# Kernel optimization log

Hardware: AMD Instinct MI355X
Metric: run time of the kernel (lower is better)

Reference implementation:

```python
import jax, jax.numpy as jnp
import numpy as np

IGNORE_INDEX = 255


def setup_inputs() -> dict:
    key = jax.random.key(0)
    k1, k2 = jax.random.split(key)
    n, h, w = 8, 256, 256
    num_class, cnum = 20, 4
    c = num_class * cnum
    P = 8192  # number of parcel segments
    features = jax.random.normal(k1, (n, c, h, w), dtype=jnp.float32)
    parcel = jax.random.randint(k2, (n, h, w), 0, P, dtype=jnp.int32)
    # all pixels of a parcel share one class label (as the torch code assumes)
    target = (parcel % num_class).astype(jnp.int32)
    return {"features": features, "target": target, "parcel": parcel,
            "num_segments": P, "cnum": cnum, "num_class": num_class}


def reference(features, target, parcel, num_segments, cnum, num_class):
    n, c, h, w = features.shape
    hw = h * w
    # n c h w -> n (h w) c
    fea = features.reshape(n, c, hw).transpose(0, 2, 1)
    # MaxPool1d(cnum, stride=cnum) over channel dim: group consecutive cnum channels
    branch_dis = fea.reshape(n, hw, num_class, cnum).max(axis=-1)  # [n, hw, num_class]
    branch_dis = branch_dis.reshape(n * hw, num_class)

    t = target.reshape(-1)
    p = parcel.reshape(-1)
    valid = t != IGNORE_INDEX
    wgt = valid.astype(branch_dis.dtype)

    # fused segment-mean replacing the python loop over unique parcel ids
    seg_sum = jax.ops.segment_sum(branch_dis * wgt[:, None], p, num_segments=num_segments)
    counts = jax.ops.segment_sum(wgt, p, num_segments=num_segments)
    seg_mean = seg_sum / jnp.maximum(counts, 1.0)[:, None]  # [P, num_class]

    # per-parcel target (labels are constant within a parcel -> max == first)
    t_masked = jnp.where(valid, t, -1)
    tgt_parcel = jax.ops.segment_max(t_masked, p, num_segments=num_segments)
    seg_valid = (counts > 0).astype(seg_mean.dtype)

    logp = jax.nn.log_softmax(seg_mean, axis=-1)
    tgt_safe = jnp.clip(tgt_parcel, 0, num_class - 1)
    nll = -jnp.take_along_axis(logp, tgt_safe[:, None], axis=1)[:, 0]
    loss_dis = jnp.sum(nll * seg_valid) / jnp.maximum(jnp.sum(seg_valid), 1.0)

    # diversity branch: softmax over spatial dim, channel-group maxpool
    branch_div = jax.nn.softmax(fea, axis=1)  # softmax over hw
    branch_div = branch_div.reshape(n, hw, num_class, cnum).max(axis=-1)
    loss_div = 1.0 - jnp.mean(jnp.sum(branch_div, axis=1)) / num_class
    return loss_dis, loss_div
```

## Files before the change

kernel.cpp:

```cpp
#include <hip/hip_runtime.h>
#include <float.h>

#define IGNORE_INDEX 255

constexpr int N_IMG = 8;
constexpr int C     = 80;
constexpr int HW    = 65536;
constexpr int NC    = 20;
constexpr int CNUM  = 4;
constexpr int P     = 8192;
constexpr int NPIX  = N_IMG * HW;
constexpr int STRIPES = 4;
constexpr int NCH   = N_IMG * C;
constexpr int ROWB  = 48;

constexpr size_t B_BDS   = 0;
constexpr size_t B_CNT   = (size_t)NPIX * ROWB;
constexpr size_t B_ACC   = B_CNT + (size_t)P * 4;
constexpr size_t B_OFF   = B_ACC + 64;
constexpr size_t B_WOFF  = B_OFF + (size_t)P * 4;
constexpr size_t B_PS    = B_WOFF + (size_t)P * 4;
constexpr size_t B_CHOFF = B_PS + (size_t)NCH * STRIPES * 4;
constexpr size_t B_TGT   = B_CHOFF + (size_t)NCH * 4;

typedef __fp16 h2v __attribute__((ext_vector_type(2)));
__device__ __forceinline__ unsigned pkh(float a, float b) {
  h2v r = __builtin_amdgcn_cvt_pkrtz(a, b);
  return __builtin_bit_cast(unsigned, r);
}
__device__ __forceinline__ void unpkh(unsigned u, float& lo, float& hi) {
  h2v r = __builtin_bit_cast(h2v, u);
  lo = (float)r.x;
  hi = (float)r.y;
}
__device__ __forceinline__ float waveSum(float v) {
#pragma unroll
  for (int o = 32; o > 0; o >>= 1) v += __shfl_down(v, o, 64);
  return v;
}

__global__ __launch_bounds__(256) void stats_hist_kernel(
    const float* __restrict__ f, const int* __restrict__ target,
    const int* __restrict__ parcel, float* __restrict__ ps,
    int* __restrict__ cnt) {
  if (blockIdx.x >= NCH * STRIPES) {
    const int t4 = (blockIdx.x - NCH * STRIPES) * 256 + threadIdx.x;
    const int4 tv = ((const int4*)target)[t4];
    const int4 pv = ((const int4*)parcel)[t4];
    if (tv.x != IGNORE_INDEX) atomicAdd(&cnt[pv.x], 1);
    if (tv.y != IGNORE_INDEX) atomicAdd(&cnt[pv.y], 1);
    if (tv.z != IGNORE_INDEX) atomicAdd(&cnt[pv.z], 1);
    if (tv.w != IGNORE_INDEX) atomicAdd(&cnt[pv.w], 1);
    return;
  }
  const int ch = blockIdx.x >> 2, stripe = blockIdx.x & 3;
  const float4* base =
      (const float4*)(f + (size_t)ch * HW + (size_t)stripe * (HW / STRIPES));
  const int n4 = HW / STRIPES / 4;
  float s = 0.f;
  for (int i = threadIdx.x; i < n4; i += 256) {
    float4 v = base[i];
    s += __expf(v.x) + __expf(v.y) + __expf(v.z) + __expf(v.w);
  }
  __shared__ float sred[4];
  const int wid = threadIdx.x >> 6, lid = threadIdx.x & 63;
  float wsv = waveSum(s);
  if (lid == 0) sred[wid] = wsv;
  __syncthreads();
  if (threadIdx.x == 0)
    ps[blockIdx.x] = sred[0] + sred[1] + sred[2] + sred[3];
}

__global__ __launch_bounds__(1024) void combine_scan_kernel(
    const float* __restrict__ ps, float* __restrict__ choff,
    const int* __restrict__ cnt, int* __restrict__ offs,
    int* __restrict__ woff) {
  const int t = threadIdx.x;
  const int lid = t & 63, wid = t >> 6;
  if (t < NCH) {
    const float4 s4 = *(const float4*)(ps + t * 4);
    choff[t] = logf(s4.x + s4.y + s4.z + s4.w);
  }
  int4 a = ((const int4*)cnt)[t * 2], b = ((const int4*)cnt)[t * 2 + 1];
  int c[8] = {a.x, a.y, a.z, a.w, b.x, b.y, b.z, b.w};
  int tot = 0;
#pragma unroll
  for (int j = 0; j < 8; j++) tot += c[j];
  int x = tot;
#pragma unroll
  for (int o = 1; o < 64; o <<= 1) {
    int y = __shfl_up(x, o, 64);
    if (lid >= o) x += y;
  }
  __shared__ int wsum[16];
  if (lid == 63) wsum[wid] = x;
  __syncthreads();
  if (t < 16) {
    int w = wsum[t];
#pragma unroll
    for (int o = 1; o < 16; o <<= 1) {
      int y = __shfl_up(w, o, 64);
      if (lid >= o) w += y;
    }
    wsum[t] = w;
  }
  __syncthreads();
  int base = (wid ? wsum[wid - 1] : 0) + (x - tot);
#pragma unroll
  for (int j = 0; j < 8; j++) {
    offs[t * 8 + j] = base;
    woff[t * 8 + j] = base;
    base += c[j];
  }
}

__global__ __launch_bounds__(256) void divbd_scatter_kernel(
    const float* __restrict__ f, const int* __restrict__ target,
    const int* __restrict__ parcel, const float* __restrict__ choff,
    int* __restrict__ woff, char* __restrict__ bdsb, int* __restrict__ tgtp,
    float* __restrict__ div_acc) {
  const int pg = blockIdx.x * 256 + threadIdx.x;
  const int img = pg >> 16;
  const int pix = pg & (HW - 1);
  const float* fb = f + (size_t)img * C * HW + pix;
  __shared__ float soff[C];
  if (threadIdx.x < C) soff[threadIdx.x] = choff[img * C + threadIdx.x];
  __syncthreads();

  float dm[NC];
  float divs = 0.f;
#pragma unroll
  for (int k = 0; k < NC; k++) {
    float d = -FLT_MAX, e = -FLT_MAX;
#pragma unroll
    for (int j = 0; j < CNUM; j++) {
      const int ch = k * CNUM + j;
      float v = fb[(size_t)ch * HW];
      d = fmaxf(d, v);
      e = fmaxf(e, v - soff[ch]);
    }
    dm[k] = d;
    divs += __expf(e);
  }

  const int t = target[pg];
  const int p = parcel[pg];
  if (t != IGNORE_INDEX) {
    const int pos = atomicAdd(&woff[p], 1);
    uint4* row = (uint4*)(bdsb + (size_t)pos * ROWB);
    row[0] = make_uint4(pkh(dm[0], dm[1]), pkh(dm[2], dm[3]),
                        pkh(dm[4], dm[5]), pkh(dm[6], dm[7]));
    row[1] = make_uint4(pkh(dm[8], dm[9]), pkh(dm[10], dm[11]),
                        pkh(dm[12], dm[13]), pkh(dm[14], dm[15]));
    row[2] = make_uint4(pkh(dm[16], dm[17]), pkh(dm[18], dm[19]), 0u, 0u);
    tgtp[p] = t;
  }

  __shared__ float sred[4];
  const int wid = threadIdx.x >> 6, lid = threadIdx.x & 63;
  float wsum = waveSum(divs);
  if (lid == 0) sred[wid] = wsum;
  __syncthreads();
  if (threadIdx.x == 0)
    atomicAdd(div_acc, sred[0] + sred[1] + sred[2] + sred[3]);
}

__global__ __launch_bounds__(256) void parcel_fin_kernel(
    const char* __restrict__ bdsb, const int* __restrict__ cnt,
    const int* __restrict__ offs, const int* __restrict__ tgtp,
    float* __restrict__ acc, float* __restrict__ out) {
  const int wid = threadIdx.x >> 6, lid = threadIdx.x & 63;
  const int p = blockIdx.x * 4 + wid;
  const int c = cnt[p];
  float sums[NC];
#pragma unroll
  for (int k = 0; k < NC; k++) sums[k] = 0.f;
  if (c > 0) {
    const int start = offs[p];
    for (int i = lid; i < c; i += 64) {
      const uint4* row = (const uint4*)(bdsb + (size_t)(start + i) * ROWB);
      uint4 r0 = row[0], r1 = row[1];
      uint2 r2 = ((const uint2*)row)[4];
      unsigned u[10] = {r0.x, r0.y, r0.z, r0.w, r1.x,
                        r1.y, r1.z, r1.w, r2.x, r2.y};
#pragma unroll
      for (int q = 0; q < 10; q++) {
        float lo, hi;
        unpkh(u[q], lo, hi);
        sums[2 * q] += lo;
        sums[2 * q + 1] += hi;
      }
    }
  }
#pragma unroll
  for (int o = 32; o > 0; o >>= 1) {
#pragma unroll
    for (int k = 0; k < NC; k++) sums[k] += __shfl_xor(sums[k], o, 64);
  }
  float nll = 0.f, val = 0.f;
  if (c > 0) {
    const float inv = 1.f / (float)c;
    float mean[NC];
    float m = -FLT_MAX;
#pragma unroll
    for (int k = 0; k < NC; k++) {
      mean[k] = sums[k] * inv;
      m = fmaxf(m, mean[k]);
    }
    float se = 0.f;
#pragma unroll
    for (int k = 0; k < NC; k++) se += __expf(mean[k] - m);
    const float lse = m + logf(se);
    const int t = min(max(tgtp[p], 0), NC - 1);
    nll = lse - mean[t];
    val = 1.f;
  }
  __shared__ float sn[4], sv[4];
  if (lid == 0) { sn[wid] = nll; sv[wid] = val; }
  __syncthreads();
  if (threadIdx.x == 0) {
    atomicAdd(&acc[1], sn[0] + sn[1] + sn[2] + sn[3]);
    atomicAdd(&acc[2], sv[0] + sv[1] + sv[2] + sv[3]);
    __threadfence();
    unsigned done = atomicAdd((unsigned*)&acc[3], 1u);
    if (done == gridDim.x - 1) {
      const float div = atomicAdd(&acc[0], 0.f);
      const float nl  = atomicAdd(&acc[1], 0.f);
      const float vc  = atomicAdd(&acc[2], 0.f);
      out[0] = nl / fmaxf(vc, 1.f);
      out[1] = 1.f - div / (float)(N_IMG * NC * NC);
    }
  }
}

extern "C" void kernel_launch(void* const* d_in, const int* in_sizes, int n_in,
                              void* d_out, int out_size, void* d_ws,
                              size_t ws_size, hipStream_t stream) {
  const float* features = (const float*)d_in[0];
  const int*   target   = (const int*)d_in[1];
  const int*   parcel   = (const int*)d_in[2];
  float* out = (float*)d_out;
  char* wsb = (char*)d_ws;
  (void)in_sizes; (void)n_in; (void)out_size; (void)ws_size;

  char*  bdsb  = wsb + B_BDS;
  int*   cnt   = (int*)(wsb + B_CNT);
  float* acc   = (float*)(wsb + B_ACC);
  int*   offs  = (int*)(wsb + B_OFF);
  int*   woff  = (int*)(wsb + B_WOFF);
  float* ps    = (float*)(wsb + B_PS);
  float* choff = (float*)(wsb + B_CHOFF);
  int*   tgtp  = (int*)(wsb + B_TGT);

  (void)hipMemsetAsync(wsb + B_CNT, 0, P * 4 + 64, stream);

  stats_hist_kernel<<<NCH * STRIPES + NPIX / 1024, 256, 0, stream>>>(
      features, target, parcel, ps, cnt);
  combine_scan_kernel<<<1, 1024, 0, stream>>>(ps, choff, cnt, offs, woff);
  divbd_scatter_kernel<<<NPIX / 256, 256, 0, stream>>>(
      features, target, parcel, choff, woff, bdsb, tgtp, acc + 0);
  parcel_fin_kernel<<<P / 4, 256, 0, stream>>>(bdsb, cnt, offs, tgtp, acc,
                                               out);
}
```

Measured before the change: 389.7 us.

## Fuse four-kernel pipeline into one persistent cooperative kernel with grid syncs

Replaces the four separate launches (stats/histogram, scan, scatter, per-parcel finalize) with a single persistent cooperative kernel of 512 blocks. Each phase is grid-strided and the phases are separated by grid.sync, and the scan now runs in one 256-thread block. The aim is to remove launch overhead and inter-kernel gaps. In exchange it caps parallelism at 512 blocks and adds grid-wide barrier costs, which may lower occupancy and latency hiding in the heavy scatter phase. The old multi-kernel path is kept as a fallback if the cooperative launch fails.

```diff
diff --git a/kernel.cpp b/kernel.cpp
--- a/kernel.cpp
+++ b/kernel.cpp
@@ -1,5 +1,8 @@
 #include <hip/hip_runtime.h>
+#include <hip/hip_cooperative_groups.h>
 #include <float.h>
+
+namespace cg = cooperative_groups;
 
 #define IGNORE_INDEX 255
 
@@ -13,6 +16,7 @@
 constexpr int STRIPES = 4;
 constexpr int NCH   = N_IMG * C;
 constexpr int ROWB  = 48;
+constexpr int GRID  = 512;
 
 constexpr size_t B_BDS   = 0;
 constexpr size_t B_CNT   = (size_t)NPIX * ROWB;
@@ -37,6 +41,202 @@
 #pragma unroll
   for (int o = 32; o > 0; o >>= 1) v += __shfl_down(v, o, 64);
   return v;
+}
+
+__global__ __launch_bounds__(256, 2) void mega_kernel(
+    const float* __restrict__ f, const int* __restrict__ target,
+    const int* __restrict__ parcel, char* __restrict__ wsb,
+    float* __restrict__ out) {
+  cg::grid_group grid = cg::this_grid();
+
+  char*  bdsb  = wsb + B_BDS;
+  int*   cnt   = (int*)(wsb + B_CNT);
+  float* acc   = (float*)(wsb + B_ACC);
+  int*   offs  = (int*)(wsb + B_OFF);
+  int*   woff  = (int*)(wsb + B_WOFF);
+  float* ps    = (float*)(wsb + B_PS);
+  float* choff = (float*)(wsb + B_CHOFF);
+  int*   tgtp  = (int*)(wsb + B_TGT);
+
+  const int tid = threadIdx.x, bid = blockIdx.x;
+  const int lid = tid & 63, wid = tid >> 6;
+  __shared__ float sred[4];
+  __shared__ float soff[C];
+  __shared__ int   ws4[4];
+
+  for (int tile = bid; tile < NCH * STRIPES + NPIX / 1024; tile += GRID) {
+    if (tile >= NCH * STRIPES) {
+      const int t4 = (tile - NCH * STRIPES) * 256 + tid;
+      const int4 tv = ((const int4*)target)[t4];
+      const int4 pv = ((const int4*)parcel)[t4];
+      if (tv.x != IGNORE_INDEX) atomicAdd(&cnt[pv.x], 1);
+      if (tv.y != IGNORE_INDEX) atomicAdd(&cnt[pv.y], 1);
+      if (tv.z != IGNORE_INDEX) atomicAdd(&cnt[pv.z], 1);
+      if (tv.w != IGNORE_INDEX) atomicAdd(&cnt[pv.w], 1);
+    } else {
+      const int ch = tile >> 2, stripe = tile & 3;
+      const float4* base = (const float4*)(f + (size_t)ch * HW +
+                                           (size_t)stripe * (HW / STRIPES));
+      const int n4 = HW / STRIPES / 4;
+      float s = 0.f;
+      for (int i = tid; i < n4; i += 256) {
+        float4 v = base[i];
+        s += __expf(v.x) + __expf(v.y) + __expf(v.z) + __expf(v.w);
+      }
+      float wsv = waveSum(s);
+      __syncthreads();
+      if (lid == 0) sred[wid] = wsv;
+      __syncthreads();
+      if (tid == 0) ps[tile] = sred[0] + sred[1] + sred[2] + sred[3];
+    }
+  }
+  grid.sync();
+
+  if (bid == 0) {
+    for (int ch = tid; ch < NCH; ch += 256) {
+      const float4 s4 = *(const float4*)(ps + ch * 4);
+      choff[ch] = logf(s4.x + s4.y + s4.z + s4.w);
+    }
+    int c[32];
+#pragma unroll
+    for (int q = 0; q < 8; q++) {
+      const int4 v = ((const int4*)cnt)[tid * 8 + q];
+      c[q * 4] = v.x; c[q * 4 + 1] = v.y; c[q * 4 + 2] = v.z;
+      c[q * 4 + 3] = v.w;
+    }
+    int tot = 0;
+#pragma unroll
+    for (int j = 0; j < 32; j++) tot += c[j];
+    int x = tot;
+#pragma unroll
+    for (int o = 1; o < 64; o <<= 1) {
+      int y = __shfl_up(x, o, 64);
+      if (lid >= o) x += y;
+    }
+    if (lid == 63) ws4[wid] = x;
+    __syncthreads();
+    int wbase = 0;
+    for (int w = 0; w < wid; w++) wbase += ws4[w];
+    int e = wbase + x - tot;
+#pragma unroll
+    for (int j = 0; j < 32; j++) {
+      offs[tid * 32 + j] = e;
+      woff[tid * 32 + j] = e;
+      e += c[j];
+    }
+  }
+  grid.sync();
+
+  for (int tile = bid; tile < NPIX / 256; tile += GRID) {
+    const int pg = tile * 256 + tid;
+    const int img = pg >> 16;
+    const int pix = pg & (HW - 1);
+    const float* fb = f + (size_t)img * C * HW + pix;
+    __syncthreads();
+    if (tid < C) soff[tid] = choff[img * C + tid];
+    __syncthreads();
+
+    float dm[NC];
+    float divs = 0.f;
+#pragma unroll
+    for (int k = 0; k < NC; k++) {
+      float d = -FLT_MAX, e = -FLT_MAX;
+#pragma unroll
+      for (int j = 0; j < CNUM; j++) {
+        const int ch = k * CNUM + j;
+        float v = fb[(size_t)ch * HW];
+        d = fmaxf(d, v);
+        e = fmaxf(e, v - soff[ch]);
+      }
+      dm[k] = d;
+      divs += __expf(e);
+    }
+
+    const int t = target[pg];
+    const int p = parcel[pg];
+    if (t != IGNORE_INDEX) {
+      const int pos = atomicAdd(&woff[p], 1);
+      uint4* row = (uint4*)(bdsb + (size_t)pos * ROWB);
+      row[0] = make_uint4(pkh(dm[0], dm[1]), pkh(dm[2], dm[3]),
+                          pkh(dm[4], dm[5]), pkh(dm[6], dm[7]));
+      row[1] = make_uint4(pkh(dm[8], dm[9]), pkh(dm[10], dm[11]),
+                          pkh(dm[12], dm[13]), pkh(dm[14], dm[15]));
+      row[2] = make_uint4(pkh(dm[16], dm[17]), pkh(dm[18], dm[19]), 0u, 0u);
+      tgtp[p] = t;
+    }
+
+    float wsum = waveSum(divs);
+    if (lid == 0) sred[wid] = wsum;
+    __syncthreads();
+    if (tid == 0)
+      atomicAdd(&acc[0], sred[0] + sred[1] + sred[2] + sred[3]);
+  }
+  grid.sync();
+
+  for (int tile = bid; tile < P / 4; tile += GRID) {
+    const int p = tile * 4 + wid;
+    const int c = cnt[p];
+    float sums[NC];
+#pragma unroll
+    for (int k = 0; k < NC; k++) sums[k] = 0.f;
+    if (c > 0) {
+      const int start = offs[p];
+      for (int i = lid; i < c; i += 64) {
+        const uint4* row = (const uint4*)(bdsb + (size_t)(start + i) * ROWB);
+        uint4 r0 = row[0], r1 = row[1];
+        uint2 r2 = ((const uint2*)row)[4];
+        unsigned u[10] = {r0.x, r0.y, r0.z, r0.w, r1.x,
+                          r1.y, r1.z, r1.w, r2.x, r2.y};
+#pragma unroll
+        for (int q = 0; q < 10; q++) {
+          float lo, hi;
+          unpkh(u[q], lo, hi);
+          sums[2 * q] += lo;
+          sums[2 * q + 1] += hi;
+        }
+      }
+    }
+#pragma unroll
+    for (int o = 32; o > 0; o >>= 1) {
+#pragma unroll
+      for (int k = 0; k < NC; k++) sums[k] += __shfl_xor(sums[k], o, 64);
+    }
+    float nll = 0.f, val = 0.f;
+    if (c > 0) {
+      const float inv = 1.f / (float)c;
+      float mean[NC];
+      float m = -FLT_MAX;
+#pragma unroll
+      for (int k = 0; k < NC; k++) {
+        mean[k] = sums[k] * inv;
+        m = fmaxf(m, mean[k]);
+      }
+      float se = 0.f;
+#pragma unroll
+      for (int k = 0; k < NC; k++) se += __expf(mean[k] - m);
+      const float lse = m + logf(se);
+      const int t = min(max(tgtp[p], 0), NC - 1);
+      nll = lse - mean[t];
+      val = 1.f;
+    }
+    __syncthreads();
+    if (lid == 0) { sred[wid] = nll; ws4[wid] = __float_as_int(val); }
+    __syncthreads();
+    if (tid == 0) {
+      atomicAdd(&acc[1], sred[0] + sred[1] + sred[2] + sred[3]);
+      atomicAdd(&acc[2], __int_as_float(ws4[0]) + __int_as_float(ws4[1]) +
+                             __int_as_float(ws4[2]) + __int_as_float(ws4[3]));
+    }
+  }
+  grid.sync();
+
+  if (bid == 0 && tid == 0) {
+    const float div = atomicAdd(&acc[0], 0.f);
+    const float nl  = atomicAdd(&acc[1], 0.f);
+    const float vc  = atomicAdd(&acc[2], 0.f);
+    out[0] = nl / fmaxf(vc, 1.f);
+    out[1] = 1.f - div / (float)(N_IMG * NC * NC);
+  }
 }
 
 __global__ __launch_bounds__(256) void stats_hist_kernel(
@@ -240,7 +440,7 @@
   const int*   target   = (const int*)d_in[1];
   const int*   parcel   = (const int*)d_in[2];
   float* out = (float*)d_out;
-  char* wsb = (char*)d_ws;
+  char*  wsb = (char*)d_ws;
   (void)in_sizes; (void)n_in; (void)out_size; (void)ws_size;
 
   char*  bdsb  = wsb + B_BDS;
@@ -254,11 +454,17 @@
 
   (void)hipMemsetAsync(wsb + B_CNT, 0, P * 4 + 64, stream);
 
-  stats_hist_kernel<<<NCH * STRIPES + NPIX / 1024, 256, 0, stream>>>(
-      features, target, parcel, ps, cnt);
-  combine_scan_kernel<<<1, 1024, 0, stream>>>(ps, choff, cnt, offs, woff);
-  divbd_scatter_kernel<<<NPIX / 256, 256, 0, stream>>>(
-      features, target, parcel, choff, woff, bdsb, tgtp, acc + 0);
-  parcel_fin_kernel<<<P / 4, 256, 0, stream>>>(bdsb, cnt, offs, tgtp, acc,
-                                               out);
-}
+  void* args[] = {(void*)&features, (void*)&target, (void*)&parcel,
+                  (void*)&wsb, (void*)&out};
+  hipError_t err = hipLaunchCooperativeKernel(
+      (void*)mega_kernel, dim3(GRID), dim3(256), args, 0, stream);
+  if (err != hipSuccess) {
+    stats_hist_kernel<<<NCH * STRIPES + NPIX / 1024, 256, 0, stream>>>(
+        features, target, parcel, ps, cnt);
+    combine_scan_kernel<<<1, 1024, 0, stream>>>(ps, choff, cnt, offs, woff);
+    divbd_scatter_kernel<<<NPIX / 256, 256, 0, stream>>>(
+        features, target, parcel, choff, woff, bdsb, tgtp, acc + 0);
+    parcel_fin_kernel<<<P / 4, 256, 0, stream>>>(bdsb, cnt, offs, tgtp, acc,
+                                                 out);
+  }
+}
```

After: 601.2 us. +54.3%, slower.
